# Kernel tuning notes

Measured on AMD Instinct MI355X. Metric: run time of the kernel, lower is better.

Reference implementation:

```python
import jax, jax.numpy as jnp
import numpy as np

B, NN, D, H, L, E, NC = 512, 64, 128, 4, 2, 262144, 8
N = B * NN
HD = D // H


def _mlp(x, W1, b1, W2, b2):
    return jax.nn.relu(x @ W1 + b1) @ W2 + b2


def setup_inputs() -> dict:
    key = jax.random.key(0)
    ks = iter(jax.random.split(key, 64))
    w = lambda shape, s=0.02: jax.random.normal(next(ks), shape, dtype=jnp.float32) * s
    inp = {
        'node_features': jax.random.randint(next(ks), (N,), 0, NC, dtype=jnp.int32),
        'edge_index': jax.random.randint(next(ks), (2, E), 0, N, dtype=jnp.int32),
        'ptr': jnp.arange(B + 1, dtype=jnp.int32) * NN,
        'node_emb_table': w((NC, D), 1.0),
        'edge_emb': jnp.clip(jax.random.normal(next(ks), (1, D), dtype=jnp.float32), -2.0, 2.0),
        'eW1': w((L, 3 * D, D)), 'eb1': jnp.zeros((L, D)), 'eW2': w((L, D, D)), 'eb2': jnp.zeros((L, D)),
        'nW1': w((L, 3 * D, D)), 'nb1': jnp.zeros((L, D)), 'nW2': w((L, D, D)), 'nb2': jnp.zeros((L, D)),
        'gW1': w((L, 3 * D, D)), 'gb1': jnp.zeros((L, D)), 'gW2': w((L, D, D)), 'gb2': jnp.zeros((L, D)),
        'projW': w((D, 3 * D)), 'projb': jnp.zeros((3 * D,)),
        'Wq': w((D, D)), 'Wk': w((D, D)), 'Wv': w((D, D)),
        'bq': jnp.zeros((D,)), 'bk': jnp.zeros((D,)), 'bv': jnp.zeros((D,)),
        'outW': w((D, D)), 'outb': jnp.zeros((D,)),
        'sW1': w((D, D)), 'sb1': jnp.zeros((D,)), 'sW2': w((D, D)), 'sb2': jnp.zeros((D,)),
        'rW1': w((D, D)), 'rb1': jnp.zeros((D,)), 'rW2': w((D, D)), 'rb2': jnp.zeros((D,)),
        'stW1': w((D, D)), 'stb1': jnp.zeros((D,)), 'stW2': w((D, 1)), 'stb2': jnp.zeros((1,)),
        'temperature': jnp.float32(1.0),
    }
    return inp


def reference(node_features, edge_index, ptr, node_emb_table, edge_emb,
              eW1, eb1, eW2, eb2, nW1, nb1, nW2, nb2, gW1, gb1, gW2, gb2,
              projW, projb, Wq, Wk, Wv, bq, bk, bv, outW, outb,
              sW1, sb1, sW2, sb2, rW1, rb1, rW2, rb2,
              stW1, stb1, stW2, stb2, temperature):
    n_graphs = ptr.shape[0] - 1                       # static
    batch_idx = jnp.repeat(jnp.arange(n_graphs), NN)  # uniform graphs of NN nodes
    node_embs = node_emb_table[node_features]         # [N, D]
    edge_embs = jnp.broadcast_to(edge_emb, (edge_index.shape[1], D))  # [E, D]
    g = jnp.zeros((n_graphs, D), node_embs.dtype)
    src, dst = edge_index[0], edge_index[1]
    for l in range(L):
        ein = jnp.concatenate([node_embs[src], node_embs[dst], edge_embs], -1)  # [E, 3D]
        edge_embs = edge_embs + _mlp(ein, eW1[l], eb1[l], eW2[l], eb2[l])
        node_aggr = jax.ops.segment_sum(edge_embs, dst, num_segments=N)         # [N, D]
        nin = jnp.concatenate([node_embs, node_aggr, g[batch_idx]], -1)
        node_embs = node_embs + _mlp(nin, nW1[l], nb1[l], nW2[l], nb2[l])
        eg = jax.ops.segment_sum(node_aggr, batch_idx, num_segments=n_graphs)
        ng = jax.ops.segment_sum(node_embs, batch_idx, num_segments=n_graphs)
        g = g + _mlp(jnp.concatenate([ng, eg, g], -1), gW1[l], gb1[l], gW2[l], gb2[l])
    # projection + self-attention over the NN nodes of each graph
    x = node_embs.reshape(n_graphs, NN, D) @ projW + projb   # [B, NN, 3D]
    q, k, v = jnp.split(x, 3, axis=-1)
    qh = (q @ Wq + bq).reshape(n_graphs, NN, H, HD)
    kh = (k @ Wk + bk).reshape(n_graphs, NN, H, HD)
    vh = (v @ Wv + bv).reshape(n_graphs, NN, H, HD)
    scores = jnp.einsum('bqhd,bkhd->bhqk', qh, kh) / jnp.sqrt(jnp.float32(HD))
    attn = jax.nn.softmax(scores, axis=-1)
    ctx = jnp.einsum('bhqk,bkhd->bqhd', attn, vh).reshape(n_graphs, NN, D)
    a = ctx @ outW + outb
    senders = _mlp(a, sW1, sb1, sW2, sb2)
    receivers = _mlp(a, rW1, rb1, rW2, rb2)
    edge_actions = jnp.einsum('bqd,bkd->bqk', senders, receivers).reshape(n_graphs, NN * NN)
    edge_actions = edge_actions / jax.nn.softplus(temperature)
    stop = _mlp(g, stW1, stb1, stW2, stb2)[:, 0]
    at = jnp.full((n_graphs, 3), -jnp.inf, dtype=edge_actions.dtype)
    at = at.at[:, 1].set(jax.nn.log_sigmoid(-stop))   # ADD_EDGE
    at = at.at[:, 2].set(jax.nn.log_sigmoid(stop))    # EXIT
    return (at, edge_actions)
```

## Files before the change

### kernel.cpp

```cpp
#include <hip/hip_runtime.h>
#include <hip/hip_bf16.h>
#include <cstdint>
#include <cstddef>

#define D_   128
#define NN_  64
#define B_   512
#define N_   32768
#define E_   262144

typedef float4 f4;
typedef _Float16 h16;
typedef __attribute__((ext_vector_type(8))) _Float16 h16x8;
typedef __attribute__((ext_vector_type(4))) float f32x4;

__device__ __forceinline__ f4 ld4(const float* p) { return *(const f4*)p; }
__device__ __forceinline__ void st4(float* p, f4 v) { *(f4*)p = v; }

__device__ __forceinline__ int swz(int row, int slot) {
  return row * 128 + ((slot ^ (row & 7)) << 3);
}
__device__ __forceinline__ h16x8 pk8(f4 a, f4 b) {
  h16x8 v;
  v[0]=(h16)a.x; v[1]=(h16)a.y; v[2]=(h16)a.z; v[3]=(h16)a.w;
  v[4]=(h16)b.x; v[5]=(h16)b.y; v[6]=(h16)b.z; v[7]=(h16)b.w;
  return v;
}
#define MFMA16(a,b,c) __builtin_amdgcn_mfma_f32_16x16x32_f16((a),(b),(c),0,0,0)

__device__ __forceinline__ void stage_a32(const float* __restrict__ A, h16* A_s, int r0, int tid) {
  int r = tid >> 2, q = tid & 3;
  const float* Ar = A + (size_t)(r0 + r) * 128 + q * 32;
#pragma unroll
  for (int i = 0; i < 4; ++i)
    *(h16x8*)&A_s[swz(r, q * 4 + i)] = pk8(ld4(Ar + i * 8), ld4(Ar + i * 8 + 4));
}
__device__ __forceinline__ void bfrag_g(const h16* __restrict__ Bt, int n0, int lq, int lr, h16x8 bf[2][4]) {
#pragma unroll
  for (int nf = 0; nf < 2; ++nf) {
    const h16* row = Bt + (size_t)(n0 + nf * 16 + lr) * 128 + lq * 8;
#pragma unroll
    for (int ks = 0; ks < 4; ++ks)
      bf[nf][ks] = *(const h16x8*)(row + ks * 32);
  }
}
__device__ __forceinline__ void mfma8(const h16* A_s, h16x8 bf[2][4], f32x4 acc[4][2], int lq, int lr) {
#pragma unroll
  for (int mf = 0; mf < 4; ++mf)
#pragma unroll
    for (int ks = 0; ks < 4; ++ks) {
      h16x8 af = *(h16x8*)&A_s[swz(mf * 16 + lr, ks * 4 + lq)];
      acc[mf][0] = MFMA16(af, bf[0][ks], acc[mf][0]);
      acc[mf][1] = MFMA16(af, bf[1][ks], acc[mf][1]);
    }
}
__device__ __forceinline__ void zacc(f32x4 acc[4][2]) {
#pragma unroll
  for (int mf = 0; mf < 4; ++mf) { acc[mf][0] = (f32x4)0.f; acc[mf][1] = (f32x4)0.f; }
}

__global__ __launch_bounds__(256)
void k_embed(const int* __restrict__ nf, const float* __restrict__ tab, float* __restrict__ out) {
  int idx = blockIdx.x * 256 + threadIdx.x;
  int row = idx >> 5, q = idx & 31;
  st4(out + (size_t)row * D_ + q * 4, ld4(tab + (size_t)nf[row] * D_ + q * 4));
}

__global__ __launch_bounds__(256)
void k_zero_cnt(int* __restrict__ cnt) { cnt[blockIdx.x * 256 + threadIdx.x] = 0; }

__global__ __launch_bounds__(256)
void k_hist(const int* __restrict__ dst, int* __restrict__ cnt) {
  atomicAdd(&cnt[dst[blockIdx.x * 256 + threadIdx.x]], 1);
}

__global__ __launch_bounds__(256)
void k_scan(const int* __restrict__ cnt, int* __restrict__ base, int* __restrict__ cursor) {
  __shared__ int sums[256];
  __shared__ int offs[256];
  const int t = threadIdx.x;
  const int start = t * 128;
  int s = 0;
  for (int i = 0; i < 128; ++i) s += cnt[start + i];
  sums[t] = s;
  __syncthreads();
  if (t == 0) { int acc = 0; for (int i = 0; i < 256; ++i) { offs[i] = acc; acc += sums[i]; } }
  __syncthreads();
  int off = offs[t];
  for (int i = 0; i < 128; ++i) { base[start + i] = off; cursor[start + i] = off; off += cnt[start + i]; }
  if (t == 255) base[N_] = off;
}

__global__ __launch_bounds__(256)
void k_scatter(const int* __restrict__ dst, int* __restrict__ cursor, int* __restrict__ eid) {
  int e = blockIdx.x * 256 + threadIdx.x;
  int p = atomicAdd(&cursor[dst[e]], 1);
  eid[p] = e;
}

__global__ __launch_bounds__(256)
void k_aggr(const h16* __restrict__ edgeb, const int* __restrict__ csrB,
            float* __restrict__ aggr) {
  const int node = blockIdx.x * 4 + (threadIdx.x >> 6);
  const int d2 = (threadIdx.x & 63) * 2;
  const int b0 = csrB[node], b1 = csrB[node + 1];
  float s0 = 0.f, s1 = 0.f;
  for (int i = b0; i < b1; ++i) {
    const h16* p = edgeb + (size_t)i * 128 + d2;
    s0 += (float)p[0]; s1 += (float)p[1];
  }
  aggr[(size_t)node * 128 + d2 + 0] = s0;
  aggr[(size_t)node * 128 + d2 + 1] = s1;
}

struct TP { const float* p[32]; };
__global__ __launch_bounds__(256)
void k_w2t(TP tp, h16* __restrict__ dst) {
  __shared__ h16 w_s[128][132];
  const float* S = tp.p[blockIdx.x];
  h16* Dd = dst + (size_t)blockIdx.x * 16384;
  const int t = threadIdx.x, r = t >> 1, hf = t & 1;
  for (int i = 0; i < 64; i += 4) {
    f4 x = ld4(S + r * 128 + hf * 64 + i);
    w_s[r][hf*64+i+0] = (h16)x.x; w_s[r][hf*64+i+1] = (h16)x.y;
    w_s[r][hf*64+i+2] = (h16)x.z; w_s[r][hf*64+i+3] = (h16)x.w;
  }
  __syncthreads();
  for (int i8 = 0; i8 < 64; i8 += 8) {
    h16x8 v;
#pragma unroll
    for (int j = 0; j < 8; ++j) v[j] = w_s[hf*64 + i8 + j][r];
    *(h16x8*)(Dd + (size_t)r * 128 + hf * 64 + i8) = v;
  }
}

__global__ __launch_bounds__(256, 2)
void k_hgemm(const float* __restrict__ A, int lda, const h16* __restrict__ Bt,
             float* __restrict__ C, const float* __restrict__ bias,
             const float* __restrict__ addC, const float* __restrict__ rowterm,
             int relu, h16* __restrict__ Ch) {
  __shared__ h16 A_s[64 * 128];
  const int tid = threadIdx.x;
  const int r0 = blockIdx.x * 64;
  {
    int r = tid >> 2, q = tid & 3;
    const float* Ar = A + (size_t)(r0 + r) * lda + q * 32;
#pragma unroll
    for (int i = 0; i < 4; ++i)
      *(h16x8*)&A_s[swz(r, q * 4 + i)] = pk8(ld4(Ar + i * 8), ld4(Ar + i * 8 + 4));
  }
  __syncthreads();
  const int lane = tid & 63, w = tid >> 6;
  const int n0 = w * 32, lq = lane >> 4, lr = lane & 15;
  h16x8 bf[2][4];
  bfrag_g(Bt, n0, lq, lr, bf);
  f32x4 acc[4][2];
  zacc(acc);
  mfma8(A_s, bf, acc, lq, lr);
#pragma unroll
  for (int nf = 0; nf < 2; ++nf) {
    const int col = n0 + nf * 16 + lr;
    const float bv = bias ? bias[col] : 0.f;
#pragma unroll
    for (int mf = 0; mf < 4; ++mf) {
      f32x4 a = acc[mf][nf];
#pragma unroll
      for (int reg = 0; reg < 4; ++reg) {
        const int row = r0 + mf * 16 + lq * 4 + reg;
        float x = a[reg] + bv;
        if (rowterm) x += rowterm[(size_t)(row >> 6) * 128 + col];
        if (addC)    x += addC[(size_t)row * 128 + col];
        if (relu)    x = fmaxf(x, 0.f);
        if (Ch) Ch[(size_t)row * 128 + col] = (h16)x;
        else    C[(size_t)row * 128 + col] = x;
      }
    }
  }
}

__global__ __launch_bounds__(256, 2)
void k_gemm3o(const float* __restrict__ A,
              const h16* __restrict__ B1, const h16* __restrict__ B2,
              const h16* __restrict__ B3,
              const float* __restrict__ bias,
              h16* __restrict__ O1, h16* __restrict__ O2, h16* __restrict__ O3) {
  __shared__ h16 A_s[64 * 128];
  const int tid = threadIdx.x;
  const int r0 = blockIdx.x * 64;
  const int lane = tid & 63, w = tid >> 6;
  const int n0 = w * 32, lq = lane >> 4, lr = lane & 15;
  stage_a32(A, A_s, r0, tid);
  __syncthreads();
  const h16* Bs[3] = {B1, B2, B3};
  h16*       Os[3] = {O1, O2, O3};
#pragma unroll
  for (int o = 0; o < 3; ++o) {
    if (!Bs[o]) break;
    h16x8 bf[2][4];
    f32x4 acc[4][2];
    bfrag_g(Bs[o], n0, lq, lr, bf);
    zacc(acc);
    mfma8(A_s, bf, acc, lq, lr);
#pragma unroll
    for (int nf = 0; nf < 2; ++nf) {
      const int col = n0 + nf * 16 + lr;
      const float bv = bias ? bias[o * 128 + col] : 0.f;
#pragma unroll
      for (int mf = 0; mf < 4; ++mf)
#pragma unroll
        for (int reg = 0; reg < 4; ++reg)
          Os[o][(size_t)(r0 + mf * 16 + lq * 4 + reg) * 128 + col] = (h16)(acc[mf][nf][reg] + bv);
    }
  }
}

__global__ __launch_bounds__(256, 2)
void k_mlp2(const float* __restrict__ A1, const float* __restrict__ A2,
            const float* __restrict__ A3,
            const h16* __restrict__ B1a, const h16* __restrict__ B1b,
            const h16* __restrict__ B1c,
            const float* __restrict__ bias1, const float* __restrict__ rowterm,
            const h16* __restrict__ B2, const float* __restrict__ bias2,
            const float* __restrict__ addC, int relu2,
            float* __restrict__ C, h16* __restrict__ Ch) {
  __shared__ h16 A_s[64 * 128];
  const int tid = threadIdx.x;
  const int r0 = blockIdx.x * 64;
  const int lane = tid & 63, w = tid >> 6;
  const int n0 = w * 32, lq = lane >> 4, lr = lane & 15;
  h16x8 bf[2][4];
  f32x4 acc[4][2];
  zacc(acc);
  stage_a32(A1, A_s, r0, tid);
  __syncthreads();
  bfrag_g(B1a, n0, lq, lr, bf);
  mfma8(A_s, bf, acc, lq, lr);
  if (A2) {
    __syncthreads();
    stage_a32(A2, A_s, r0, tid);
    __syncthreads();
    bfrag_g(B1b, n0, lq, lr, bf);
    mfma8(A_s, bf, acc, lq, lr);
  }
  if (A3) {
    __syncthreads();
    stage_a32(A3, A_s, r0, tid);
    __syncthreads();
    bfrag_g(B1c, n0, lq, lr, bf);
    mfma8(A_s, bf, acc, lq, lr);
  }
  __syncthreads();
  const int g = r0 >> 6;
#pragma unroll
  for (int nf = 0; nf < 2; ++nf) {
    const int col = n0 + nf * 16 + lr;
    float b1v = bias1 ? bias1[col] : 0.f;
    if (rowterm) b1v += rowterm[(size_t)g * 128 + col];
#pragma unroll
    for (int mf = 0; mf < 4; ++mf)
#pragma unroll
      for (int reg = 0; reg < 4; ++reg) {
        const int row = mf * 16 + lq * 4 + reg;
        A_s[swz(row, col >> 3) + (col & 7)] = (h16)fmaxf(acc[mf][nf][reg] + b1v, 0.f);
      }
  }
  __syncthreads();
  bfrag_g(B2, n0, lq, lr, bf);
  zacc(acc);
  mfma8(A_s, bf, acc, lq, lr);
#pragma unroll
  for (int nf = 0; nf < 2; ++nf) {
    const int col = n0 + nf * 16 + lr;
    const float b2v = bias2 ? bias2[col] : 0.f;
#pragma unroll
    for (int mf = 0; mf < 4; ++mf)
#pragma unroll
      for (int reg = 0; reg < 4; ++reg) {
        const int row = r0 + mf * 16 + lq * 4 + reg;
        float x = acc[mf][nf][reg] + b2v;
        if (addC) x += addC[(size_t)row * 128 + col];
        if (relu2) x = fmaxf(x, 0.f);
        if (Ch) Ch[(size_t)row * 128 + col] = (h16)x;
        else    C[(size_t)row * 128 + col] = x;
      }
  }
}

__global__ __launch_bounds__(256, 2)
void k_mlp2d(const float* __restrict__ A,
             const h16* __restrict__ B1a, const float* __restrict__ b1a,
             const h16* __restrict__ B2a, const float* __restrict__ b2a, h16* __restrict__ O1,
             const h16* __restrict__ B1b, const float* __restrict__ b1b,
             const h16* __restrict__ B2b, const float* __restrict__ b2b, h16* __restrict__ O2) {
  __shared__ h16 A_s[64 * 128];
  __shared__ h16 H_s[64 * 128];
  const int tid = threadIdx.x, r0 = blockIdx.x * 64;
  const int lane = tid & 63, w = tid >> 6;
  const int n0 = w * 32, lq = lane >> 4, lr = lane & 15;
  stage_a32(A, A_s, r0, tid);
  __syncthreads();
  const h16* W1[2] = {B1a, B1b};
  const h16* W2[2] = {B2a, B2b};
  const float* bb1[2] = {b1a, b1b};
  const float* bb2[2] = {b2a, b2b};
  h16* OO[2] = {O1, O2};
#pragma unroll
  for (int c = 0; c < 2; ++c) {
    h16x8 bf[2][4];
    f32x4 acc[4][2];
    bfrag_g(W1[c], n0, lq, lr, bf);
    zacc(acc);
    mfma8(A_s, bf, acc, lq, lr);
#pragma unroll
    for (int nf = 0; nf < 2; ++nf) {
      const int col = n0 + nf * 16 + lr;
      const float b1v = bb1[c][col];
#pragma unroll
      for (int mf = 0; mf < 4; ++mf)
#pragma unroll
        for (int reg = 0; reg < 4; ++reg) {
          const int row = mf * 16 + lq * 4 + reg;
          H_s[swz(row, col >> 3) + (col & 7)] = (h16)fmaxf(acc[mf][nf][reg] + b1v, 0.f);
        }
    }
    __syncthreads();
    bfrag_g(W2[c], n0, lq, lr, bf);
    zacc(acc);
    mfma8(H_s, bf, acc, lq, lr);
#pragma unroll
    for (int nf = 0; nf < 2; ++nf) {
      const int col = n0 + nf * 16 + lr;
      const float b2v = bb2[c][col];
#pragma unroll
      for (int mf = 0; mf < 4; ++mf)
#pragma unroll
        for (int reg = 0; reg < 4; ++reg)
          OO[c][(size_t)(r0 + mf * 16 + lq * 4 + reg) * 128 + col] = (h16)(acc[mf][nf][reg] + b2v);
    }
    __syncthreads();
  }
}

__global__ __launch_bounds__(128)
void k_hc0(const float* __restrict__ ee, const float* __restrict__ W1c,
           const float* __restrict__ b1, float* __restrict__ hc0) {
  int j = threadIdx.x;
  float s = b1[j];
  for (int d = 0; d < 128; ++d) s += ee[d] * W1c[d * 128 + j];
  hc0[j] = s;
}

__global__ __launch_bounds__(256, 2)
void k_edge0(const int* __restrict__ src, const int* __restrict__ dst,
             const int* __restrict__ eid,
             const h16* __restrict__ hs, const h16* __restrict__ hd,
             const float* __restrict__ hc0, const h16* __restrict__ Wt2,
             const float* __restrict__ eb2, const float* __restrict__ ee,
             h16* __restrict__ edgeb) {
  __shared__ h16 H_s[64 * 128];
  __shared__ int ss[64], sd[64];
  const int tid = threadIdx.x;
  const int bid = (blockIdx.x & 7) * (E_ / 64 / 8) + (blockIdx.x >> 3);
  const int e0 = bid * 64;
  const int lane = tid & 63, w = tid >> 6;
  const int n0 = w * 32, lq = lane >> 4, lr = lane & 15;
  if (tid < 64) { int e = eid[e0 + tid]; ss[tid] = src[e]; sd[tid] = dst[e]; }
  __syncthreads();
  {
    int e = tid >> 2, q = tid & 3;
    const h16* ps = hs + (size_t)ss[e] * 128 + q * 32;
    const h16* pd = hd + (size_t)sd[e] * 128 + q * 32;
#pragma unroll
    for (int i = 0; i < 4; ++i) {
      h16x8 a = *(const h16x8*)(ps + i * 8);
      h16x8 b = *(const h16x8*)(pd + i * 8);
      f4 c0 = ld4(hc0 + q * 32 + i * 8), c1 = ld4(hc0 + q * 32 + i * 8 + 4);
      h16x8 v;
      v[0]=(h16)fmaxf((float)a[0]+(float)b[0]+c0.x,0.f); v[1]=(h16)fmaxf((float)a[1]+(float)b[1]+c0.y,0.f);
      v[2]=(h16)fmaxf((float)a[2]+(float)b[2]+c0.z,0.f); v[3]=(h16)fmaxf((float)a[3]+(float)b[3]+c0.w,0.f);
      v[4]=(h16)fmaxf((float)a[4]+(float)b[4]+c1.x,0.f); v[5]=(h16)fmaxf((float)a[5]+(float)b[5]+c1.y,0.f);
      v[6]=(h16)fmaxf((float)a[6]+(float)b[6]+c1.z,0.f); v[7]=(h16)fmaxf((float)a[7]+(float)b[7]+c1.w,0.f);
      *(h16x8*)&H_s[swz(e, q * 4 + i)] = v;
    }
  }
  __syncthreads();
  h16x8 bf[2][4];
  f32x4 acc[4][2];
  bfrag_g(Wt2, n0, lq, lr, bf);
  zacc(acc);
  mfma8(H_s, bf, acc, lq, lr);
  __syncthreads();
#pragma unroll
  for (int nf = 0; nf < 2; ++nf) {
    const int col = n0 + nf * 16 + lr;
    const float base = eb2[col] + ee[col];
#pragma unroll
    for (int mf = 0; mf < 4; ++mf)
#pragma unroll
      for (int reg = 0; reg < 4; ++reg) {
        const int row = mf * 16 + lq * 4 + reg;
        H_s[swz(row, col >> 3) + (col & 7)] = (h16)(acc[mf][nf][reg] + base);
      }
  }
  __syncthreads();
  {
    int r = tid >> 2, q = tid & 3;
#pragma unroll
    for (int i = 0; i < 4; ++i) {
      int slot = q * 4 + i;
      h16x8 v = *(const h16x8*)&H_s[swz(r, slot)];
      *(h16x8*)(edgeb + (size_t)(e0 + r) * 128 + slot * 8) = v;
    }
  }
}

__global__ __launch_bounds__(256, 2)
void k_edge1(const int* __restrict__ src, const int* __restrict__ dst,
             const int* __restrict__ eid,
             h16* __restrict__ edgeb,
             const h16* __restrict__ hs, const h16* __restrict__ hd,
             const h16* __restrict__ Wt1c, const float* __restrict__ b1,
             const h16* __restrict__ Wt2, const float* __restrict__ b2) {
  __shared__ h16 T_s[64 * 128];
  __shared__ h16 HS_s[64 * 128];
  __shared__ int ss[64], sd[64];
  const int tid = threadIdx.x;
  const int bid = (blockIdx.x & 7) * (E_ / 64 / 8) + (blockIdx.x >> 3);
  const int e0 = bid * 64;
  const int lane = tid & 63, w = tid >> 6;
  const int n0 = w * 32, lq = lane >> 4, lr = lane & 15;
  if (tid < 64) { int e = eid[e0 + tid]; ss[tid] = src[e]; sd[tid] = dst[e]; }
  {
    int r = tid >> 2, q = tid & 3;
    const h16* Er = edgeb + (size_t)(e0 + r) * 128 + q * 32;
#pragma unroll
    for (int i = 0; i < 4; ++i)
      *(h16x8*)&T_s[swz(r, q * 4 + i)] = *(const h16x8*)(Er + i * 8);
  }
  __syncthreads();
  {
    int e = tid >> 2, q = tid & 3;
    const h16* ps = hs + (size_t)ss[e] * 128 + q * 32;
    const h16* pd = hd + (size_t)sd[e] * 128 + q * 32;
#pragma unroll
    for (int i = 0; i < 4; ++i) {
      h16x8 a = *(const h16x8*)(ps + i * 8);
      h16x8 b = *(const h16x8*)(pd + i * 8);
      f4 c0 = ld4(b1 + q * 32 + i * 8), c1 = ld4(b1 + q * 32 + i * 8 + 4);
      h16x8 v;
      v[0]=(h16)((float)a[0]+(float)b[0]+c0.x); v[1]=(h16)((float)a[1]+(float)b[1]+c0.y);
      v[2]=(h16)((float)a[2]+(float)b[2]+c0.z); v[3]=(h16)((float)a[3]+(float)b[3]+c0.w);
      v[4]=(h16)((float)a[4]+(float)b[4]+c1.x); v[5]=(h16)((float)a[5]+(float)b[5]+c1.y);
      v[6]=(h16)((float)a[6]+(float)b[6]+c1.z); v[7]=(h16)((float)a[7]+(float)b[7]+c1.w);
      *(h16x8*)&HS_s[swz(e, q * 4 + i)] = v;
    }
  }
  h16x8 bf[2][4];
  f32x4 acc[4][2];
  bfrag_g(Wt1c, n0, lq, lr, bf);
  zacc(acc);
  mfma8(T_s, bf, acc, lq, lr);
  float rres[2][4][4];
#pragma unroll
  for (int nf = 0; nf < 2; ++nf) {
    const int col = n0 + nf * 16 + lr;
#pragma unroll
    for (int mf = 0; mf < 4; ++mf)
#pragma unroll
      for (int reg = 0; reg < 4; ++reg) {
        const int row = mf * 16 + lq * 4 + reg;
        rres[nf][mf][reg] = (float)T_s[swz(row, col >> 3) + (col & 7)];
      }
  }
  __syncthreads();
#pragma unroll
  for (int nf = 0; nf < 2; ++nf) {
    const int col = n0 + nf * 16 + lr;
#pragma unroll
    for (int mf = 0; mf < 4; ++mf)
#pragma unroll
      for (int reg = 0; reg < 4; ++reg) {
        const int row = mf * 16 + lq * 4 + reg;
        float x = acc[mf][nf][reg] + (float)HS_s[swz(row, col >> 3) + (col & 7)];
        T_s[swz(row, col >> 3) + (col & 7)] = (h16)fmaxf(x, 0.f);
      }
  }
  __syncthreads();
  bfrag_g(Wt2, n0, lq, lr, bf);
  zacc(acc);
  mfma8(T_s, bf, acc, lq, lr);
#pragma unroll
  for (int nf = 0; nf < 2; ++nf) {
    const int col = n0 + nf * 16 + lr;
    const float b2v = b2[col];
#pragma unroll
    for (int mf = 0; mf < 4; ++mf)
#pragma unroll
      for (int reg = 0; reg < 4; ++reg) {
        const int row = mf * 16 + lq * 4 + reg;
        HS_s[swz(row, col >> 3) + (col & 7)] = (h16)(acc[mf][nf][reg] + b2v + rres[nf][mf][reg]);
      }
  }
  __syncthreads();
  {
    int r = tid >> 2, q = tid & 3;
#pragma unroll
    for (int i = 0; i < 4; ++i) {
      int slot = q * 4 + i;
      h16x8 v = *(const h16x8*)&HS_s[swz(r, slot)];
      *(h16x8*)(edgeb + (size_t)(e0 + r) * 128 + slot * 8) = v;
    }
  }
}

__global__ __launch_bounds__(128)
void k_rowsum2(const float* __restrict__ X1, const float* __restrict__ X2,
               float* __restrict__ Y1, float* __restrict__ Y2) {
  int b = blockIdx.x, d = threadIdx.x;
  float s1 = 0.f, s2 = 0.f;
#pragma unroll 8
  for (int r = 0; r < 64; ++r) {
    s1 += X1[((size_t)b * 64 + r) * 128 + d];
    s2 += X2[((size_t)b * 64 + r) * 128 + d];
  }
  Y1[b * 128 + d] = s1;
  Y2[b * 128 + d] = s2;
}

__global__ __launch_bounds__(128)
void k_beff(const float* __restrict__ projb,
            const float* __restrict__ Wq, const float* __restrict__ Wk, const float* __restrict__ Wv,
            const float* __restrict__ bq, const float* __restrict__ bk, const float* __restrict__ bv,
            float* __restrict__ beff) {
  int i = blockIdx.x, k = threadIdx.x;
  const float* W = (i == 0) ? Wq : ((i == 1) ? Wk : Wv);
  const float* bb = (i == 0) ? bq : ((i == 1) ? bk : bv);
  float s = bb[k];
  for (int j = 0; j < 128; ++j) s += projb[i * 128 + j] * W[j * 128 + k];
  beff[i * 128 + k] = s;
}

__global__ __launch_bounds__(256, 2)
void k_attn(const h16* __restrict__ Q, const h16* __restrict__ K,
            const h16* __restrict__ V, float* __restrict__ ctx) {
  __shared__ h16 k_s[64][136];
  __shared__ h16 v_s[64][136];
  const int tid = threadIdx.x, b = blockIdx.x;
  const size_t base = (size_t)b * 64 * 128;
  {
    int r = tid >> 2, q = tid & 3;
#pragma unroll
    for (int i = 0; i < 4; ++i) {
      *(h16x8*)&k_s[r][q * 32 + i * 8] = *(const h16x8*)(K + base + r * 128 + q * 32 + i * 8);
      *(h16x8*)&v_s[r][q * 32 + i * 8] = *(const h16x8*)(V + base + r * 128 + q * 32 + i * 8);
    }
  }
  __syncthreads();
  const int w = tid >> 6, lane = tid & 63, co = w * 32;
  h16x8 qv[4];
#pragma unroll
  for (int j = 0; j < 4; ++j)
    qv[j] = *(const h16x8*)(Q + base + (size_t)lane * 128 + co + j * 8);
  float s[64];
  const float scale = 0.17677669529663688f;
#pragma unroll 8
  for (int k = 0; k < 64; ++k) {
    float a = 0.f;
#pragma unroll
    for (int j = 0; j < 4; ++j) {
      h16x8 k8 = *(const h16x8*)&k_s[k][co + j * 8];
#pragma unroll
      for (int t = 0; t < 8; ++t) a += (float)qv[j][t] * (float)k8[t];
    }
    s[k] = a * scale;
  }
  float m = s[0];
#pragma unroll
  for (int k = 1; k < 64; ++k) m = fmaxf(m, s[k]);
  float sum = 0.f;
#pragma unroll
  for (int k = 0; k < 64; ++k) { s[k] = expf(s[k] - m); sum += s[k]; }
  const float inv = 1.f / sum;
  f4 cv[8];
#pragma unroll
  for (int jj = 0; jj < 8; ++jj) cv[jj] = make_float4(0.f, 0.f, 0.f, 0.f);
#pragma unroll 4
  for (int k = 0; k < 64; ++k) {
    float p = s[k];
#pragma unroll
    for (int j = 0; j < 4; ++j) {
      h16x8 v8 = *(const h16x8*)&v_s[k][co + j * 8];
      cv[2*j].x   += p * (float)v8[0]; cv[2*j].y   += p * (float)v8[1];
      cv[2*j].z   += p * (float)v8[2]; cv[2*j].w   += p * (float)v8[3];
      cv[2*j+1].x += p * (float)v8[4]; cv[2*j+1].y += p * (float)v8[5];
      cv[2*j+1].z += p * (float)v8[6]; cv[2*j+1].w += p * (float)v8[7];
    }
  }
#pragma unroll
  for (int j = 0; j < 8; ++j) {
    f4 t = cv[j];
    t.x *= inv; t.y *= inv; t.z *= inv; t.w *= inv;
    st4(ctx + base + (size_t)lane * 128 + co + j * 4, t);
  }
}

__global__ __launch_bounds__(256, 2)
void k_edgeact(const h16* __restrict__ S, const h16* __restrict__ R,
               const float* __restrict__ temp, float* __restrict__ out) {
  __shared__ h16 S_s[64 * 128];
  const int tid = threadIdx.x;
  const int b = blockIdx.x;
  const size_t base = (size_t)b * 64 * 128;
  {
    int r = tid >> 2, q = tid & 3;
#pragma unroll
    for (int i = 0; i < 4; ++i)
      *(h16x8*)&S_s[swz(r, q * 4 + i)] = *(const h16x8*)(S + base + r * 128 + (q * 4 + i) * 8);
  }
  __syncthreads();
  const int lane = tid & 63, w = tid >> 6;
  const int n0 = w * 16, lq = lane >> 4, lr = lane & 15;
  h16x8 bf[4];
#pragma unroll
  for (int ks = 0; ks < 4; ++ks)
    bf[ks] = *(const h16x8*)(R + base + (size_t)(n0 + lr) * 128 + lq * 8 + ks * 32);
  f32x4 acc[4];
#pragma unroll
  for (int mf = 0; mf < 4; ++mf) acc[mf] = (f32x4)0.f;
#pragma unroll
  for (int mf = 0; mf < 4; ++mf)
#pragma unroll
    for (int ks = 0; ks < 4; ++ks) {
      h16x8 af = *(h16x8*)&S_s[swz(mf * 16 + lr, ks * 4 + lq)];
      acc[mf] = MFMA16(af, bf[ks], acc[mf]);
    }
  const float inv = 1.f / log1pf(expf(temp[0]));
  __syncthreads();
  float* O_s = (float*)S_s;
#pragma unroll
  for (int mf = 0; mf < 4; ++mf)
#pragma unroll
    for (int reg = 0; reg < 4; ++reg)
      O_s[(mf * 16 + lq * 4 + reg) * 64 + n0 + lr] = acc[mf][reg] * inv;
  __syncthreads();
#pragma unroll
  for (int i = 0; i < 4; ++i)
    st4(out + (size_t)b * 4096 + tid * 16 + i * 4, *(const f4*)&O_s[tid * 16 + i * 4]);
}

__global__ __launch_bounds__(256)
void k_stop_at(const float* __restrict__ gh, const float* __restrict__ stW2,
               const float* __restrict__ stb2, float* __restrict__ out) {
  int b = blockIdx.x * 256 + threadIdx.x;
  if (b >= B_) return;
  float s = stb2[0];
  for (int j = 0; j < 128; ++j) s += gh[(size_t)b * 128 + j] * stW2[j];
  float l = log1pf(expf(-fabsf(s)));
  out[b * 3 + 0] = -3.3895313892515355e38f;
  out[b * 3 + 1] = fminf(-s, 0.f) - l;
  out[b * 3 + 2] = fminf(s, 0.f) - l;
}

static const size_t OFF_NODE  = 0;
static const size_t OFF_HSRC  = 4194304;
static const size_t OFF_HDST  = 8388608;
static const size_t OFF_AGGR  = 12582912;
static const size_t OFF_HID   = 16777216;
static const size_t OFF_G     = 20971520;
static const size_t OFF_GTERM = OFF_G + 65536;
static const size_t OFF_GH    = OFF_GTERM + 65536;
static const size_t OFF_NG    = OFF_GH + 65536;
static const size_t OFF_EG    = OFF_NG + 65536;
static const size_t OFF_WEFF  = OFF_EG + 65536;
static const size_t OFF_BEFF  = OFF_WEFF + 49152;
static const size_t OFF_HC0   = OFF_BEFF + 384;
static const size_t OFF_EDGE  = 21495808;
static const size_t OFF_CSR   = OFF_EDGE + (size_t)E_ * 128;
static const size_t CSR_INTS  = (size_t)N_ + (N_ + 1) + N_ + E_;
static const size_t OFF_WT    = OFF_CSR + ((CSR_INTS + 63) & ~(size_t)63) / 1 / 4 * 4 + 64;

#define WT_WQ 0
#define WT_WK 1
#define WT_WV 2
#define WT_OUTW 3
#define WT_SW1 4
#define WT_SW2 5
#define WT_RW1 6
#define WT_RW2 7
#define WT_STW1 8
#define WT_L(l,i) (9 + (l)*11 + (i))
#define WT_EW1C1 31
#define WT_WEFF 32
#define WTP(i) (wt + (size_t)(i) * 16384)

static inline void hgemm(hipStream_t st, const float* A, int lda, const h16* Bt, int M,
                         float* C, const float* bias, const float* addC,
                         const float* rowterm, int relu, h16* Ch) {
  k_hgemm<<<M / 64, 256, 0, st>>>(A, lda, Bt, C, bias, addC, rowterm, relu, Ch);
}

extern "C" void kernel_launch(void* const* d_in, const int* in_sizes, int n_in,
                              void* d_out, int out_size, void* d_ws, size_t ws_size,
                              hipStream_t stream) {
  (void)in_sizes; (void)n_in; (void)out_size; (void)ws_size;
  const int*   nf    = (const int*)d_in[0];
  const int*   ei    = (const int*)d_in[1];
  const float* tab   = (const float*)d_in[3];
  const float* ee    = (const float*)d_in[4];
  const float* eW1   = (const float*)d_in[5];
  const float* eb1   = (const float*)d_in[6];
  const float* eW2   = (const float*)d_in[7];
  const float* eb2   = (const float*)d_in[8];
  const float* nW1   = (const float*)d_in[9];
  const float* nb1   = (const float*)d_in[10];
  const float* nW2   = (const float*)d_in[11];
  const float* nb2   = (const float*)d_in[12];
  const float* gW1   = (const float*)d_in[13];
  const float* gb1   = (const float*)d_in[14];
  const float* gW2   = (const float*)d_in[15];
  const float* gb2   = (const float*)d_in[16];
  const float* projW = (const float*)d_in[17];
  const float* projb = (const float*)d_in[18];
  const float* Wq    = (const float*)d_in[19];
  const float* Wk    = (const float*)d_in[20];
  const float* Wv    = (const float*)d_in[21];
  const float* bq    = (const float*)d_in[22];
  const float* bk    = (const float*)d_in[23];
  const float* bv    = (const float*)d_in[24];
  const float* outW  = (const float*)d_in[25];
  const float* outb  = (const float*)d_in[26];
  const float* sW1   = (const float*)d_in[27];
  const float* sb1   = (const float*)d_in[28];
  const float* sW2   = (const float*)d_in[29];
  const float* sb2   = (const float*)d_in[30];
  const float* rW1   = (const float*)d_in[31];
  const float* rb1   = (const float*)d_in[32];
  const float* rW2   = (const float*)d_in[33];
  const float* rb2   = (const float*)d_in[34];
  const float* stW1  = (const float*)d_in[35];
  const float* stb1  = (const float*)d_in[36];
  const float* stW2  = (const float*)d_in[37];
  const float* stb2  = (const float*)d_in[38];
  const float* temp  = (const float*)d_in[39];

  const int* srcI = ei;
  const int* dstI = ei + E_;

  float* ws    = (float*)d_ws;
  float* node  = ws + OFF_NODE;
  float* hsrcF = ws + OFF_HSRC;
  float* hdstF = ws + OFF_HDST;
  float* aggr  = ws + OFF_AGGR;
  float* hid   = ws + OFF_HID;
  float* gbuf  = ws + OFF_G;
  float* gterm = ws + OFF_GTERM;
  float* gh    = ws + OFF_GH;
  float* ngb   = ws + OFF_NG;
  float* egb   = ws + OFF_EG;
  float* weff  = ws + OFF_WEFF;
  float* beff  = ws + OFF_BEFF;
  float* hc0   = ws + OFF_HC0;
  h16*  hsrcH  = (h16*)hsrcF;
  h16*  hdstH  = (h16*)hdstF;
  h16*  vH     = (h16*)hid;
  h16*  edgebH = (h16*)(ws + OFF_EDGE);
  int* cnt    = (int*)(ws + OFF_CSR);
  int* csrB   = cnt + N_;
  int* cursor = csrB + (N_ + 1);
  int* eidL   = cursor + N_;
  h16* wt     = (h16*)(ws + OFF_WT);
  float* outp = (float*)d_out;

  hipMemsetAsync(gbuf, 0, (size_t)B_ * D_ * sizeof(float), stream);
  k_embed<<<4096, 256, 0, stream>>>(nf, tab, node);

  k_zero_cnt<<<N_ / 256, 256, 0, stream>>>(cnt);
  k_hist<<<E_ / 256, 256, 0, stream>>>(dstI, cnt);
  k_scan<<<1, 256, 0, stream>>>(cnt, csrB, cursor);
  k_scatter<<<E_ / 256, 256, 0, stream>>>(dstI, cursor, eidL);

  TP tp;
  tp.p[WT_WQ] = Wq; tp.p[WT_WK] = Wk; tp.p[WT_WV] = Wv; tp.p[WT_OUTW] = outW;
  tp.p[WT_SW1] = sW1; tp.p[WT_SW2] = sW2; tp.p[WT_RW1] = rW1; tp.p[WT_RW2] = rW2;
  tp.p[WT_STW1] = stW1;
  for (int l = 0; l < 2; ++l) {
    tp.p[WT_L(l,0)]  = eW1 + (size_t)l * 384 * 128;
    tp.p[WT_L(l,1)]  = eW1 + (size_t)l * 384 * 128 + 128 * 128;
    tp.p[WT_L(l,2)]  = eW2 + (size_t)l * 128 * 128;
    tp.p[WT_L(l,3)]  = nW1 + (size_t)l * 384 * 128;
    tp.p[WT_L(l,4)]  = nW1 + (size_t)l * 384 * 128 + 128 * 128;
    tp.p[WT_L(l,5)]  = nW1 + (size_t)l * 384 * 128 + 256 * 128;
    tp.p[WT_L(l,6)]  = nW2 + (size_t)l * 128 * 128;
    tp.p[WT_L(l,7)]  = gW1 + (size_t)l * 384 * 128;
    tp.p[WT_L(l,8)]  = gW1 + (size_t)l * 384 * 128 + 128 * 128;
    tp.p[WT_L(l,9)]  = gW1 + (size_t)l * 384 * 128 + 256 * 128;
    tp.p[WT_L(l,10)] = gW2 + (size_t)l * 128 * 128;
  }
  tp.p[WT_EW1C1] = eW1 + (size_t)384 * 128 + 256 * 128;
  k_w2t<<<32, 256, 0, stream>>>(tp, wt);

  hgemm(stream, projW + 0,   384, WTP(WT_WQ), 128, weff + 0,     nullptr, nullptr, nullptr, 0, nullptr);
  hgemm(stream, projW + 128, 384, WTP(WT_WK), 128, weff + 16384, nullptr, nullptr, nullptr, 0, nullptr);
  hgemm(stream, projW + 256, 384, WTP(WT_WV), 128, weff + 32768, nullptr, nullptr, nullptr, 0, nullptr);
  TP tp2;
  tp2.p[0] = weff; tp2.p[1] = weff + 16384; tp2.p[2] = weff + 32768;
  k_w2t<<<3, 256, 0, stream>>>(tp2, wt + (size_t)WT_WEFF * 16384);
  k_beff<<<3, 128, 0, stream>>>(projb, Wq, Wk, Wv, bq, bk, bv, beff);

  for (int l = 0; l < 2; ++l) {
    const float* eb1l = eb1 + l * 128;
    const float* eb2l = eb2 + l * 128;
    const float* nb1l = nb1 + l * 128;
    const float* nb2l = nb2 + l * 128;
    const float* gb1l = gb1 + l * 128;
    const float* gb2l = gb2 + l * 128;

    k_gemm3o<<<N_ / 64, 256, 0, stream>>>(node, WTP(WT_L(l,0)), WTP(WT_L(l,1)), nullptr,
                                          nullptr, hsrcH, hdstH, nullptr);
    if (l == 0) {
      k_hc0<<<1, 128, 0, stream>>>(ee, eW1 + 256 * 128, eb1l, hc0);
      k_edge0<<<E_ / 64, 256, 0, stream>>>(srcI, dstI, eidL, hsrcH, hdstH, hc0,
                                           WTP(WT_L(0,2)), eb2l, ee, edgebH);
    } else {
      k_edge1<<<E_ / 64, 256, 0, stream>>>(srcI, dstI, eidL, edgebH, hsrcH, hdstH,
                                           WTP(WT_EW1C1), eb1l, WTP(WT_L(1,2)), eb2l);
    }
    k_aggr<<<N_ / 4, 256, 0, stream>>>(edgebH, csrB, aggr);
    hgemm(stream, gbuf, 128, WTP(WT_L(l,5)), B_, gterm, nb1l, nullptr, nullptr, 0, nullptr);
    k_mlp2<<<N_ / 64, 256, 0, stream>>>(node, aggr, nullptr,
                                        WTP(WT_L(l,3)), WTP(WT_L(l,4)), nullptr,
                                        nullptr, gterm,
                                        WTP(WT_L(l,6)), nb2l, node, 0, node, nullptr);
    k_rowsum2<<<B_, 128, 0, stream>>>(node, aggr, ngb, egb);
    k_mlp2<<<B_ / 64, 256, 0, stream>>>(ngb, egb, gbuf,
                                        WTP(WT_L(l,7)), WTP(WT_L(l,8)), WTP(WT_L(l,9)),
                                        gb1l, nullptr,
                                        WTP(WT_L(l,10)), gb2l, gbuf, 0, gbuf, nullptr);
  }

  k_gemm3o<<<N_ / 64, 256, 0, stream>>>(node, WTP(WT_WEFF + 0), WTP(WT_WEFF + 1), WTP(WT_WEFF + 2),
                                        beff, hsrcH, hdstH, vH);
  k_attn<<<B_, 256, 0, stream>>>(hsrcH, hdstH, vH, aggr);
  hgemm(stream, aggr, 128, WTP(WT_OUTW), N_, node, outb, nullptr, nullptr, 0, nullptr);
  k_mlp2d<<<N_ / 64, 256, 0, stream>>>(node,
                                       WTP(WT_SW1), sb1, WTP(WT_SW2), sb2, hsrcH,
                                       WTP(WT_RW1), rb1, WTP(WT_RW2), rb2, hdstH);
  k_edgeact<<<B_, 256, 0, stream>>>(hsrcH, hdstH, temp, outp + 3 * B_);
  hgemm(stream, gbuf, 128, WTP(WT_STW1), B_, gh, stb1, nullptr, nullptr, 1, nullptr);
  k_stop_at<<<2, 256, 0, stream>>>(gh, stW2, stb2, outp);
}
```

Baseline: 519.1 us.

## Fuse node MLP with graph sums, attention with output projection, and stop head

Merges the per-layer gterm GEMM, node MLP and rowsum kernels into one per-graph kernel that also computes the node and edge graph sums. It folds the attention output projection into the attention kernel, fuses the stop-head MLP, and computes the effective QKV weights directly in transposed half precision. The edge kernels also drop their block-index swizzle. Together these cut kernel launches and intermediate global round trips, at the cost of more shared memory per block and a naive scalar g-term dot product inside the node kernel.

```diff
diff --git a/kernel.cpp b/kernel.cpp
--- a/kernel.cpp
+++ b/kernel.cpp
@@ -34,6 +34,13 @@
 #pragma unroll
   for (int i = 0; i < 4; ++i)
     *(h16x8*)&A_s[swz(r, q * 4 + i)] = pk8(ld4(Ar + i * 8), ld4(Ar + i * 8 + 4));
+}
+__device__ __forceinline__ void stage_a16(const h16* __restrict__ A, h16* A_s, int r0, int tid) {
+  int r = tid >> 2, q = tid & 3;
+  const h16* Ar = A + (size_t)(r0 + r) * 128 + q * 32;
+#pragma unroll
+  for (int i = 0; i < 4; ++i)
+    *(h16x8*)&A_s[swz(r, q * 4 + i)] = *(const h16x8*)(Ar + i * 8);
 }
 __device__ __forceinline__ void bfrag_g(const h16* __restrict__ Bt, int n0, int lq, int lr, h16x8 bf[2][4]) {
 #pragma unroll
@@ -135,46 +142,37 @@
 }
 
 __global__ __launch_bounds__(256, 2)
-void k_hgemm(const float* __restrict__ A, int lda, const h16* __restrict__ Bt,
-             float* __restrict__ C, const float* __restrict__ bias,
-             const float* __restrict__ addC, const float* __restrict__ rowterm,
-             int relu, h16* __restrict__ Ch) {
+void k_weff(const float* __restrict__ projW, const h16* __restrict__ wt_qkv,
+            h16* __restrict__ wout) {
   __shared__ h16 A_s[64 * 128];
+  const int i = blockIdx.x >> 1, half = blockIdx.x & 1;
+  const int r0 = half * 64;
   const int tid = threadIdx.x;
-  const int r0 = blockIdx.x * 64;
-  {
-    int r = tid >> 2, q = tid & 3;
-    const float* Ar = A + (size_t)(r0 + r) * lda + q * 32;
-#pragma unroll
-    for (int i = 0; i < 4; ++i)
-      *(h16x8*)&A_s[swz(r, q * 4 + i)] = pk8(ld4(Ar + i * 8), ld4(Ar + i * 8 + 4));
-  }
-  __syncthreads();
   const int lane = tid & 63, w = tid >> 6;
   const int n0 = w * 32, lq = lane >> 4, lr = lane & 15;
+  stage_a16(wt_qkv + (size_t)i * 16384, A_s, r0, tid);
+  __syncthreads();
   h16x8 bf[2][4];
-  bfrag_g(Bt, n0, lq, lr, bf);
+#pragma unroll
+  for (int nf = 0; nf < 2; ++nf) {
+    const int r = n0 + nf * 16 + lr;
+    const float* prow = projW + (size_t)r * 384 + i * 128 + lq * 8;
+#pragma unroll
+    for (int ks = 0; ks < 4; ++ks)
+      bf[nf][ks] = pk8(ld4(prow + ks * 32), ld4(prow + ks * 32 + 4));
+  }
   f32x4 acc[4][2];
   zacc(acc);
   mfma8(A_s, bf, acc, lq, lr);
-#pragma unroll
-  for (int nf = 0; nf < 2; ++nf) {
-    const int col = n0 + nf * 16 + lr;
-    const float bv = bias ? bias[col] : 0.f;
-#pragma unroll
-    for (int mf = 0; mf < 4; ++mf) {
-      f32x4 a = acc[mf][nf];
-#pragma unroll
-      for (int reg = 0; reg < 4; ++reg) {
-        const int row = r0 + mf * 16 + lq * 4 + reg;
-        float x = a[reg] + bv;
-        if (rowterm) x += rowterm[(size_t)(row >> 6) * 128 + col];
-        if (addC)    x += addC[(size_t)row * 128 + col];
-        if (relu)    x = fmaxf(x, 0.f);
-        if (Ch) Ch[(size_t)row * 128 + col] = (h16)x;
-        else    C[(size_t)row * 128 + col] = x;
-      }
-    }
+  h16* Wo = wout + (size_t)i * 16384;
+#pragma unroll
+  for (int nf = 0; nf < 2; ++nf) {
+    const int r = n0 + nf * 16 + lr;
+#pragma unroll
+    for (int mf = 0; mf < 4; ++mf)
+#pragma unroll
+      for (int reg = 0; reg < 4; ++reg)
+        Wo[(size_t)(r0 + mf * 16 + lq * 4 + reg) * 128 + r] = (h16)acc[mf][nf][reg];
   }
 }
 
@@ -219,10 +217,10 @@
             const float* __restrict__ A3,
             const h16* __restrict__ B1a, const h16* __restrict__ B1b,
             const h16* __restrict__ B1c,
-            const float* __restrict__ bias1, const float* __restrict__ rowterm,
+            const float* __restrict__ bias1,
             const h16* __restrict__ B2, const float* __restrict__ bias2,
-            const float* __restrict__ addC, int relu2,
-            float* __restrict__ C, h16* __restrict__ Ch) {
+            const float* __restrict__ addC,
+            float* __restrict__ C) {
   __shared__ h16 A_s[64 * 128];
   const int tid = threadIdx.x;
   const int r0 = blockIdx.x * 64;
@@ -250,12 +248,10 @@
     mfma8(A_s, bf, acc, lq, lr);
   }
   __syncthreads();
-  const int g = r0 >> 6;
 #pragma unroll
   for (int nf = 0; nf < 2; ++nf) {
     const int col = n0 + nf * 16 + lr;
-    float b1v = bias1 ? bias1[col] : 0.f;
-    if (rowterm) b1v += rowterm[(size_t)g * 128 + col];
+    const float b1v = bias1 ? bias1[col] : 0.f;
 #pragma unroll
     for (int mf = 0; mf < 4; ++mf)
 #pragma unroll
@@ -279,10 +275,86 @@
         const int row = r0 + mf * 16 + lq * 4 + reg;
         float x = acc[mf][nf][reg] + b2v;
         if (addC) x += addC[(size_t)row * 128 + col];
-        if (relu2) x = fmaxf(x, 0.f);
-        if (Ch) Ch[(size_t)row * 128 + col] = (h16)x;
-        else    C[(size_t)row * 128 + col] = x;
+        C[(size_t)row * 128 + col] = x;
       }
+  }
+}
+
+__global__ __launch_bounds__(256, 2)
+void k_nodemlp(float* __restrict__ node, const float* __restrict__ aggr,
+               const float* __restrict__ gbuf,
+               const h16* __restrict__ B1a, const h16* __restrict__ B1b,
+               const float* __restrict__ nW1c, const float* __restrict__ nb1,
+               const h16* __restrict__ B2, const float* __restrict__ nb2,
+               float* __restrict__ ngb, float* __restrict__ egb) {
+  __shared__ h16 A_s[64 * 128];
+  __shared__ float gt_s[2][128];
+  __shared__ float eg_s[2][128];
+  const int tid = threadIdx.x, g = blockIdx.x, r0 = g * 64;
+  const int lane = tid & 63, w = tid >> 6;
+  const int n0 = w * 32, lq = lane >> 4, lr = lane & 15;
+  h16x8 bf[2][4];
+  f32x4 acc[4][2];
+  zacc(acc);
+  stage_a32(node, A_s, r0, tid);
+  __syncthreads();
+  bfrag_g(B1a, n0, lq, lr, bf);
+  mfma8(A_s, bf, acc, lq, lr);
+  {
+    const int col = tid & 127, half = tid >> 7;
+    float s = 0.f;
+    const float* gb = gbuf + (size_t)g * 128;
+    for (int j = half * 64; j < half * 64 + 64; ++j)
+      s += gb[j] * nW1c[(size_t)j * 128 + col];
+    gt_s[half][col] = s;
+  }
+  __syncthreads();
+  stage_a32(aggr, A_s, r0, tid);
+  __syncthreads();
+  bfrag_g(B1b, n0, lq, lr, bf);
+  mfma8(A_s, bf, acc, lq, lr);
+  {
+    const int col = tid & 127, half = tid >> 7;
+    float s = 0.f;
+    for (int r = half * 32; r < half * 32 + 32; ++r)
+      s += aggr[((size_t)r0 + r) * 128 + col];
+    eg_s[half][col] = s;
+  }
+  __syncthreads();
+#pragma unroll
+  for (int nf = 0; nf < 2; ++nf) {
+    const int col = n0 + nf * 16 + lr;
+    const float gt = gt_s[0][col] + gt_s[1][col] + nb1[col];
+#pragma unroll
+    for (int mf = 0; mf < 4; ++mf)
+#pragma unroll
+      for (int reg = 0; reg < 4; ++reg) {
+        const int row = mf * 16 + lq * 4 + reg;
+        A_s[swz(row, col >> 3) + (col & 7)] = (h16)fmaxf(acc[mf][nf][reg] + gt, 0.f);
+      }
+  }
+  if (tid < 128) egb[(size_t)g * 128 + tid] = eg_s[0][tid] + eg_s[1][tid];
+  __syncthreads();
+  bfrag_g(B2, n0, lq, lr, bf);
+  zacc(acc);
+  mfma8(A_s, bf, acc, lq, lr);
+#pragma unroll
+  for (int nf = 0; nf < 2; ++nf) {
+    const int col = n0 + nf * 16 + lr;
+    const float b2v = nb2[col];
+    float cs = 0.f;
+#pragma unroll
+    for (int mf = 0; mf < 4; ++mf)
+#pragma unroll
+      for (int reg = 0; reg < 4; ++reg) {
+        const int row = r0 + mf * 16 + lq * 4 + reg;
+        float x = acc[mf][nf][reg] + b2v + node[(size_t)row * 128 + col];
+        node[(size_t)row * 128 + col] = x;
+        cs += x;
+      }
+    cs += __shfl_xor(cs, 16);
+    cs += __shfl_xor(cs, 32);
+    if (lq == 0) ngb[(size_t)g * 128 + col] = cs;
   }
 }
 
@@ -360,8 +432,7 @@
   __shared__ h16 H_s[64 * 128];
   __shared__ int ss[64], sd[64];
   const int tid = threadIdx.x;
-  const int bid = (blockIdx.x & 7) * (E_ / 64 / 8) + (blockIdx.x >> 3);
-  const int e0 = bid * 64;
+  const int e0 = blockIdx.x * 64;
   const int lane = tid & 63, w = tid >> 6;
   const int n0 = w * 32, lq = lane >> 4, lr = lane & 15;
   if (tid < 64) { int e = eid[e0 + tid]; ss[tid] = src[e]; sd[tid] = dst[e]; }
@@ -425,8 +496,7 @@
   __shared__ h16 HS_s[64 * 128];
   __shared__ int ss[64], sd[64];
   const int tid = threadIdx.x;
-  const int bid = (blockIdx.x & 7) * (E_ / 64 / 8) + (blockIdx.x >> 3);
-  const int e0 = bid * 64;
+  const int e0 = blockIdx.x * 64;
   const int lane = tid & 63, w = tid >> 6;
   const int n0 = w * 32, lq = lane >> 4, lr = lane & 15;
   if (tid < 64) { int e = eid[e0 + tid]; ss[tid] = src[e]; sd[tid] = dst[e]; }
@@ -511,20 +581,6 @@
       *(h16x8*)(edgeb + (size_t)(e0 + r) * 128 + slot * 8) = v;
     }
   }
-}
-
-__global__ __launch_bounds__(128)
-void k_rowsum2(const float* __restrict__ X1, const float* __restrict__ X2,
-               float* __restrict__ Y1, float* __restrict__ Y2) {
-  int b = blockIdx.x, d = threadIdx.x;
-  float s1 = 0.f, s2 = 0.f;
-#pragma unroll 8
-  for (int r = 0; r < 64; ++r) {
-    s1 += X1[((size_t)b * 64 + r) * 128 + d];
-    s2 += X2[((size_t)b * 64 + r) * 128 + d];
-  }
-  Y1[b * 128 + d] = s1;
-  Y2[b * 128 + d] = s2;
 }
 
 __global__ __launch_bounds__(128)
@@ -542,11 +598,13 @@
 
 __global__ __launch_bounds__(256, 2)
 void k_attn(const h16* __restrict__ Q, const h16* __restrict__ K,
-            const h16* __restrict__ V, float* __restrict__ ctx) {
+            const h16* __restrict__ V, const h16* __restrict__ outWt,
+            const float* __restrict__ outb, float* __restrict__ nodeOut) {
   __shared__ h16 k_s[64][136];
   __shared__ h16 v_s[64][136];
-  const int tid = threadIdx.x, b = blockIdx.x;
-  const size_t base = (size_t)b * 64 * 128;
+  __shared__ h16 A_s[64 * 128];
+  const int tid = threadIdx.x, blk = blockIdx.x;
+  const size_t base = (size_t)blk * 64 * 128;
   {
     int r = tid >> 2, q = tid & 3;
 #pragma unroll
@@ -597,10 +655,28 @@
     }
   }
 #pragma unroll
-  for (int j = 0; j < 8; ++j) {
-    f4 t = cv[j];
-    t.x *= inv; t.y *= inv; t.z *= inv; t.w *= inv;
-    st4(ctx + base + (size_t)lane * 128 + co + j * 4, t);
+  for (int jj = 0; jj < 4; ++jj) {
+    f4 a = cv[2*jj], b = cv[2*jj+1];
+    a.x *= inv; a.y *= inv; a.z *= inv; a.w *= inv;
+    b.x *= inv; b.y *= inv; b.z *= inv; b.w *= inv;
+    *(h16x8*)&A_s[swz(lane, (co >> 3) + jj)] = pk8(a, b);
+  }
+  __syncthreads();
+  const int n0 = w * 32, lq = lane >> 4, lr = lane & 15;
+  h16x8 bf[2][4];
+  f32x4 acc[4][2];
+  bfrag_g(outWt, n0, lq, lr, bf);
+  zacc(acc);
+  mfma8(A_s, bf, acc, lq, lr);
+#pragma unroll
+  for (int nf = 0; nf < 2; ++nf) {
+    const int col = n0 + nf * 16 + lr;
+    const float bv = outb[col];
+#pragma unroll
+    for (int mf = 0; mf < 4; ++mf)
+#pragma unroll
+      for (int reg = 0; reg < 4; ++reg)
+        nodeOut[base + (size_t)(mf * 16 + lq * 4 + reg) * 128 + col] = acc[mf][nf][reg] + bv;
   }
 }
 
@@ -648,17 +724,45 @@
     st4(out + (size_t)b * 4096 + tid * 16 + i * 4, *(const f4*)&O_s[tid * 16 + i * 4]);
 }
 
-__global__ __launch_bounds__(256)
-void k_stop_at(const float* __restrict__ gh, const float* __restrict__ stW2,
-               const float* __restrict__ stb2, float* __restrict__ out) {
-  int b = blockIdx.x * 256 + threadIdx.x;
-  if (b >= B_) return;
-  float s = stb2[0];
-  for (int j = 0; j < 128; ++j) s += gh[(size_t)b * 128 + j] * stW2[j];
-  float l = log1pf(expf(-fabsf(s)));
-  out[b * 3 + 0] = -3.3895313892515355e38f;
-  out[b * 3 + 1] = fminf(-s, 0.f) - l;
-  out[b * 3 + 2] = fminf(s, 0.f) - l;
+__global__ __launch_bounds__(256, 2)
+void k_stophead(const float* __restrict__ gbuf, const h16* __restrict__ stW1t,
+                const float* __restrict__ stb1, const float* __restrict__ stW2,
+                const float* __restrict__ stb2, float* __restrict__ out) {
+  __shared__ h16 A_s[64 * 128];
+  __shared__ h16 H_s[64 * 128];
+  const int tid = threadIdx.x, r0 = blockIdx.x * 64;
+  const int lane = tid & 63, w = tid >> 6;
+  const int n0 = w * 32, lq = lane >> 4, lr = lane & 15;
+  stage_a32(gbuf, A_s, r0, tid);
+  __syncthreads();
+  h16x8 bf[2][4];
+  f32x4 acc[4][2];
+  bfrag_g(stW1t, n0, lq, lr, bf);
+  zacc(acc);
+  mfma8(A_s, bf, acc, lq, lr);
+#pragma unroll
+  for (int nf = 0; nf < 2; ++nf) {
+    const int col = n0 + nf * 16 + lr;
+    const float b1v = stb1[col];
+#pragma unroll
+    for (int mf = 0; mf < 4; ++mf)
+#pragma unroll
+      for (int reg = 0; reg < 4; ++reg) {
+        const int row = mf * 16 + lq * 4 + reg;
+        H_s[swz(row, col >> 3) + (col & 7)] = (h16)fmaxf(acc[mf][nf][reg] + b1v, 0.f);
+      }
+  }
+  __syncthreads();
+  if (tid < 64) {
+    float s = stb2[0];
+    for (int c = 0; c < 128; ++c)
+      s += (float)H_s[swz(tid, c >> 3) + (c & 7)] * stW2[c];
+    float l = log1pf(expf(-fabsf(s)));
+    int b = r0 + tid;
+    out[b * 3 + 0] = -3.3895313892515355e38f;
+    out[b * 3 + 1] = fminf(-s, 0.f) - l;
+    out[b * 3 + 2] = fminf(s, 0.f) - l;
+  }
 }
 
 static const size_t OFF_NODE  = 0;
@@ -667,12 +771,9 @@
 static const size_t OFF_AGGR  = 12582912;
 static const size_t OFF_HID   = 16777216;
 static const size_t OFF_G     = 20971520;
-static const size_t OFF_GTERM = OFF_G + 65536;
-static const size_t OFF_GH    = OFF_GTERM + 65536;
-static const size_t OFF_NG    = OFF_GH + 65536;
+static const size_t OFF_NG    = OFF_G + 65536;
 static const size_t OFF_EG    = OFF_NG + 65536;
-static const size_t OFF_WEFF  = OFF_EG + 65536;
-static const size_t OFF_BEFF  = OFF_WEFF + 49152;
+static const size_t OFF_BEFF  = OFF_EG + 65536;
 static const size_t OFF_HC0   = OFF_BEFF + 384;
 static const size_t OFF_EDGE  = 21495808;
 static const size_t OFF_CSR   = OFF_EDGE + (size_t)E_ * 128;
@@ -692,12 +793,6 @@
 #define WT_EW1C1 31
 #define WT_WEFF 32
 #define WTP(i) (wt + (size_t)(i) * 16384)
-
-static inline void hgemm(hipStream_t st, const float* A, int lda, const h16* Bt, int M,
-                         float* C, const float* bias, const float* addC,
-                         const float* rowterm, int relu, h16* Ch) {
-  k_hgemm<<<M / 64, 256, 0, st>>>(A, lda, Bt, C, bias, addC, rowterm, relu, Ch);
-}
 
 extern "C" void kernel_launch(void* const* d_in, const int* in_sizes, int n_in,
                               void* d_out, int out_size, void* d_ws, size_t ws_size,
@@ -753,11 +848,8 @@
   float* aggr  = ws + OFF_AGGR;
   float* hid   = ws + OFF_HID;
   float* gbuf  = ws + OFF_G;
-  float* gterm = ws + OFF_GTERM;
-  float* gh    = ws + OFF_GH;
   float* ngb   = ws + OFF_NG;
   float* egb   = ws + OFF_EG;
-  float* weff  = ws + OFF_WEFF;
   float* beff  = ws + OFF_BEFF;
   float* hc0   = ws + OFF_HC0;
   h16*  hsrcH  = (h16*)hsrcF;
@@ -799,12 +891,7 @@
   tp.p[WT_EW1C1] = eW1 + (size_t)384 * 128 + 256 * 128;
   k_w2t<<<32, 256, 0, stream>>>(tp, wt);
 
-  hgemm(stream, projW + 0,   384, WTP(WT_WQ), 128, weff + 0,     nullptr, nullptr, nullptr, 0, nullptr);
-  hgemm(stream, projW + 128, 384, WTP(WT_WK), 128, weff + 16384, nullptr, nullptr, nullptr, 0, nullptr);
-  hgemm(stream, projW + 256, 384, WTP(WT_WV), 128, weff + 32768, nullptr, nullptr, nullptr, 0, nullptr);
-  TP tp2;
-  tp2.p[0] = weff; tp2.p[1] = weff + 16384; tp2.p[2] = weff + 32768;
-  k_w2t<<<3, 256, 0, stream>>>(tp2, wt + (size_t)WT_WEFF * 16384);
+  k_weff<<<6, 256, 0, stream>>>(projW, WTP(WT_WQ), WTP(WT_WEFF));
   k_beff<<<3, 128, 0, stream>>>(projb, Wq, Wk, Wv, bq, bk, bv, beff);
 
   for (int l = 0; l < 2; ++l) {
@@ -814,6 +901,7 @@
     const float* nb2l = nb2 + l * 128;
     const float* gb1l = gb1 + l * 128;
     const float* gb2l = gb2 + l * 128;
+    const float* nW1cl = nW1 + (size_t)l * 384 * 128 + 256 * 128;
 
     k_gemm3o<<<N_ / 64, 256, 0, stream>>>(node, WTP(WT_L(l,0)), WTP(WT_L(l,1)), nullptr,
                                           nullptr, hsrcH, hdstH, nullptr);
@@ -826,26 +914,22 @@
                                            WTP(WT_EW1C1), eb1l, WTP(WT_L(1,2)), eb2l);
     }
     k_aggr<<<N_ / 4, 256, 0, stream>>>(edgebH, csrB, aggr);
-    hgemm(stream, gbuf, 128, WTP(WT_L(l,5)), B_, gterm, nb1l, nullptr, nullptr, 0, nullptr);
-    k_mlp2<<<N_ / 64, 256, 0, stream>>>(node, aggr, nullptr,
-                                        WTP(WT_L(l,3)), WTP(WT_L(l,4)), nullptr,
-                                        nullptr, gterm,
-                                        WTP(WT_L(l,6)), nb2l, node, 0, node, nullptr);
-    k_rowsum2<<<B_, 128, 0, stream>>>(node, aggr, ngb, egb);
+    k_nodemlp<<<B_, 256, 0, stream>>>(node, aggr, gbuf,
+                                      WTP(WT_L(l,3)), WTP(WT_L(l,4)),
+                                      nW1cl, nb1l,
+                                      WTP(WT_L(l,6)), nb2l, ngb, egb);
     k_mlp2<<<B_ / 64, 256, 0, stream>>>(ngb, egb, gbuf,
                                         WTP(WT_L(l,7)), WTP(WT_L(l,8)), WTP(WT_L(l,9)),
-                                        gb1l, nullptr,
-                                        WTP(WT_L(l,10)), gb2l, gbuf, 0, gbuf, nullptr);
+                                        gb1l,
+                                        WTP(WT_L(l,10)), gb2l, gbuf, gbuf);
   }
 
   k_gemm3o<<<N_ / 64, 256, 0, stream>>>(node, WTP(WT_WEFF + 0), WTP(WT_WEFF + 1), WTP(WT_WEFF + 2),
                                         beff, hsrcH, hdstH, vH);
-  k_attn<<<B_, 256, 0, stream>>>(hsrcH, hdstH, vH, aggr);
-  hgemm(stream, aggr, 128, WTP(WT_OUTW), N_, node, outb, nullptr, nullptr, 0, nullptr);
+  k_attn<<<B_, 256, 0, stream>>>(hsrcH, hdstH, vH, WTP(WT_OUTW), outb, node);
   k_mlp2d<<<N_ / 64, 256, 0, stream>>>(node,
                                        WTP(WT_SW1), sb1, WTP(WT_SW2), sb2, hsrcH,
                                        WTP(WT_RW1), rb1, WTP(WT_RW2), rb2, hdstH);
   k_edgeact<<<B_, 256, 0, stream>>>(hsrcH, hdstH, temp, outp + 3 * B_);
-  hgemm(stream, gbuf, 128, WTP(WT_STW1), B_, gh, stb1, nullptr, nullptr, 1, nullptr);
-  k_stop_at<<<2, 256, 0, stream>>>(gh, stW2, stb2, outp);
-}
+  k_stophead<<<B_ / 64, 256, 0, stream>>>(gbuf, WTP(WT_STW1), stb1, stW2, stb2, outp);
+}
```

Measured after the change: 451.5 us. 13.0% less time.
